# Kernel optimization log

Measured on AMD Instinct MI355X. Metric: run time of the kernel, lower is better.

Reference implementation:

```python
import jax, jax.numpy as jnp
import numpy as np
import math

N_HEADS = 32
N_KV_HEADS = 8
HEAD_DIM = 64
ROPE_BASE = 10000.0


def _rope_cos_sin(L, dtype):
    # inv_freq: [head_dim/2]
    inv_freq = 1.0 / (ROPE_BASE ** (jnp.arange(0, HEAD_DIM, 2, dtype=jnp.float32) / HEAD_DIM))
    t = jnp.arange(L, dtype=jnp.float32)
    freqs = jnp.outer(t, inv_freq)            # [L, head_dim/2]
    emb = jnp.concatenate([freqs, freqs], -1)  # [L, head_dim]
    return jnp.cos(emb).astype(dtype), jnp.sin(emb).astype(dtype)


def _rotate_half(x):
    x1, x2 = jnp.split(x, 2, axis=-1)
    return jnp.concatenate([-x2, x1], axis=-1)


def setup_inputs() -> dict:
    key = jax.random.key(0)
    ks = jax.random.split(key, 5)
    B, L, D = 2, 2048, 2048
    s = 0.02
    return {
        "x": jax.random.normal(ks[0], (B, L, D), jnp.float32),
        "Wq": jax.random.normal(ks[1], (D, N_HEADS * HEAD_DIM), jnp.float32) * s,
        "Wk": jax.random.normal(ks[2], (D, N_KV_HEADS * HEAD_DIM), jnp.float32) * s,
        "Wv": jax.random.normal(ks[3], (D, N_KV_HEADS * HEAD_DIM), jnp.float32) * s,
        "Wo": jax.random.normal(ks[4], (N_HEADS * HEAD_DIM, D), jnp.float32) * s,
    }


def reference(x, Wq, Wk, Wv, Wo):
    B, L, D = x.shape
    G = N_HEADS // N_KV_HEADS
    # QKV projections -> [B, H, L, hd]
    q = (x @ Wq).reshape(B, L, N_HEADS, HEAD_DIM).transpose(0, 2, 1, 3)
    k = (x @ Wk).reshape(B, L, N_KV_HEADS, HEAD_DIM).transpose(0, 2, 1, 3)
    v = (x @ Wv).reshape(B, L, N_KV_HEADS, HEAD_DIM).transpose(0, 2, 1, 3)
    # RoPE
    cos, sin = _rope_cos_sin(L, x.dtype)  # [L, hd]
    cos = cos[None, None]
    sin = sin[None, None]
    q = q * cos + _rotate_half(q) * sin
    k = k * cos + _rotate_half(k) * sin
    # GQA expand kv heads (repeat_interleave along head dim)
    k = jnp.repeat(k, G, axis=1)
    v = jnp.repeat(v, G, axis=1)
    # Causal SDPA
    scale = 1.0 / math.sqrt(HEAD_DIM)
    scores = jnp.einsum('bhqd,bhkd->bhqk', q, k) * scale  # [B,H,L,L]
    causal = jnp.tril(jnp.ones((L, L), bool))
    scores = jnp.where(causal[None, None], scores, jnp.finfo(scores.dtype).min)
    probs = jax.nn.softmax(scores, axis=-1)
    out = jnp.einsum('bhqk,bhkd->bhqd', probs, v)  # [B,H,L,hd]
    out = out.transpose(0, 2, 1, 3).reshape(B, L, N_HEADS * HEAD_DIM)
    return out @ Wo
```

## Files before the change

### kernel.cpp

```cpp
#include <hip/hip_runtime.h>
#include <hip/hip_bf16.h>
#include <stdint.h>

typedef __bf16 bf16_t;
typedef bf16_t bf16x2 __attribute__((ext_vector_type(2)));
typedef bf16_t bf16x4 __attribute__((ext_vector_type(4)));
typedef bf16_t bf16x8 __attribute__((ext_vector_type(8)));
typedef float f32x4 __attribute__((ext_vector_type(4)));
typedef float f32x16 __attribute__((ext_vector_type(16)));

#define NH 32
#define NKV 8
#define HD 64
#define LSEQ 2048
#define DMODEL 2048
#define BATCH 2

#define QSCALE 0.18033688011112042f
#define DEFER_THR 11.5f

__device__ __forceinline__ void gl_lds16(const void* g, void* l) {
  __builtin_amdgcn_global_load_lds(
      (__attribute__((address_space(1))) char*)(uintptr_t)g,
      (__attribute__((address_space(3))) char*)(uintptr_t)l, 16, 0, 0);
}

__device__ __forceinline__ unsigned pack2(float a, float b) {
  bf16x2 t;
  t[0] = (bf16_t)a;
  t[1] = (bf16_t)b;
  return __builtin_bit_cast(unsigned, t);
}


__global__ void cvt_x(const float4* __restrict__ s, bf16x4* __restrict__ d, int n4) {
  int i = blockIdx.x * blockDim.x + threadIdx.x;
  if (i >= n4) return;
  float4 v = s[i];
  bf16x4 o;
  o[0] = (bf16_t)v.x; o[1] = (bf16_t)v.y; o[2] = (bf16_t)v.z; o[3] = (bf16_t)v.w;
  d[i] = o;
}

__global__ void transpose_w(const float* __restrict__ W, bf16_t* __restrict__ WT,
                            int K, int N) {
  __shared__ float tile[32][33];
  int nb = blockIdx.x * 32, kb = blockIdx.y * 32;
  int tx = threadIdx.x, ty = threadIdx.y;
#pragma unroll
  for (int i = 0; i < 32; i += 8)
    tile[ty + i][tx] = W[(size_t)(kb + ty + i) * N + nb + tx];
  __syncthreads();
#pragma unroll
  for (int i = 0; i < 32; i += 8)
    WT[(size_t)(nb + ty + i) * K + kb + tx] = (bf16_t)tile[tx][ty + i];
}

__global__ void rope_table(float* __restrict__ cosT, float* __restrict__ sinT) {
  int t = blockIdx.x * blockDim.x + threadIdx.x;
  int l = t >> 5, i = t & 31;
  float inv = powf(10000.0f, -(float)i / 32.0f);
  float ang = (float)l * inv;
  float s, c;
  sincosf(ang, &s, &c);
  cosT[t] = c;
  sinT[t] = s;
}

template <int EPI>
__global__ __launch_bounds__(256, 3) void gemm128(
    const bf16_t* __restrict__ A, const bf16_t* __restrict__ BT,
    float* __restrict__ Cf, bf16_t* __restrict__ Qo, bf16_t* __restrict__ Ko,
    bf16_t* __restrict__ Vo, int M, int N, int K,
    const float* __restrict__ cosT, const float* __restrict__ sinT, int nx) {
  __shared__ bf16_t Al[128 * 64];
  __shared__ bf16_t Bl[128 * 64];
  const int tid = threadIdx.x, lane = tid & 63, w = tid >> 6;
  const int wm = w >> 1, wn = w & 1;
  const int r15 = lane & 15, g = lane >> 4;
  const int nwg = (int)gridDim.x;
  const int sid = ((int)blockIdx.x & 7) * (nwg >> 3) + ((int)blockIdx.x >> 3);
  const int m0 = (sid / nx) * 128, n0 = (sid % nx) * 128;
  f32x4 acc[4][4] = {};

  for (int kt = 0; kt < K; kt += 64) {
#pragma unroll
    for (int i = 0; i < 4; ++i) {
      const int c = i * 256 + tid;
      const int row = c >> 3, cc = c & 7;
      const int sc = (cc ^ (row & 7)) * 8;
      gl_lds16(A + (size_t)(m0 + row) * K + kt + sc, Al + c * 8);
      gl_lds16(BT + (size_t)(n0 + row) * K + kt + sc, Bl + c * 8);
    }
    __syncthreads();
#pragma unroll
    for (int kk = 0; kk < 2; ++kk) {
      bf16x8 af[4], bfr[4];
#pragma unroll
      for (int mi = 0; mi < 4; ++mi) {
        const int r = wm * 64 + mi * 16 + r15;
        af[mi] = *(const bf16x8*)((const char*)Al + r * 128 +
                                  (((kk * 4 + g) ^ (r & 7)) << 4));
      }
#pragma unroll
      for (int ni = 0; ni < 4; ++ni) {
        const int r = wn * 64 + ni * 16 + r15;
        bfr[ni] = *(const bf16x8*)((const char*)Bl + r * 128 +
                                   (((kk * 4 + g) ^ (r & 7)) << 4));
      }
#pragma unroll
      for (int mi = 0; mi < 4; ++mi)
#pragma unroll
        for (int ni = 0; ni < 4; ++ni)
          acc[mi][ni] = __builtin_amdgcn_mfma_f32_16x16x32_bf16(
              af[mi], bfr[ni], acc[mi][ni], 0, 0, 0);
    }
    __syncthreads();
  }

  if constexpr (EPI == 0) {
#pragma unroll
    for (int mi = 0; mi < 4; ++mi) {
      const int row = m0 + wm * 64 + mi * 16 + g * 4;
#pragma unroll
      for (int ni = 0; ni < 4; ++ni) {
        const int col = n0 + wn * 64 + ni * 16 + r15;
#pragma unroll
        for (int r = 0; r < 4; ++r)
          Cf[(size_t)(row + r) * N + col] = acc[mi][ni][r];
      }
    }
  } else {
    const int colbase = n0 + wn * 64;
    auto rope_store = [&](bf16_t* C, int NHT, int colrel, float sc) {
#pragma unroll
      for (int mi = 0; mi < 4; ++mi)
#pragma unroll
        for (int r = 0; r < 4; ++r) {
          const int rowg = m0 + wm * 64 + mi * 16 + g * 4 + r;
          const int bb = rowg >> 11, ls = rowg & (LSEQ - 1);
#pragma unroll
          for (int ni = 0; ni < 2; ++ni) {
            const int col = colrel + ni * 16 + r15;
            const int hh = col >> 6, d = col & 63;
            const float c = cosT[ls * 32 + d], s = sinT[ls * 32 + d];
            const float v0 = acc[mi][ni][r], v1 = acc[mi][ni + 2][r];
            bf16_t* dst = C + (((size_t)bb * NHT + hh) * LSEQ + ls) * HD + d;
            dst[0] = (bf16_t)((v0 * c - v1 * s) * sc);
            dst[32] = (bf16_t)((v1 * c + v0 * s) * sc);
          }
        }
    };
    if (n0 < 2048) {
      rope_store(Qo, NH, colbase, QSCALE);
    } else if (n0 < 2560) {
      rope_store(Ko, NKV, colbase - 2048, 1.0f);
    } else {
#pragma unroll
      for (int mi = 0; mi < 4; ++mi)
#pragma unroll
        for (int r = 0; r < 4; ++r) {
          const int rowg = m0 + wm * 64 + mi * 16 + g * 4 + r;
          const int bb = rowg >> 11, ls = rowg & (LSEQ - 1);
#pragma unroll
          for (int ni = 0; ni < 4; ++ni) {
            const int col = colbase - 2560 + ni * 16 + r15;
            const int hh = col >> 6, d = col & 63;
            Vo[(((size_t)bb * NKV + hh) * HD + d) * LSEQ + ls] =
                (bf16_t)acc[mi][ni][r];
          }
        }
    }
  }
}

__global__ __launch_bounds__(256, 2) void attn_fwd(
    const bf16_t* __restrict__ Q, const bf16_t* __restrict__ Kh,
    const bf16_t* __restrict__ VTh, bf16_t* __restrict__ AO) {
  __shared__ bf16_t Kl[2][64 * 64];
  __shared__ bf16_t Vl[2][64 * 64];
  const int tid = threadIdx.x, lane = tid & 63, w = tid >> 6;
  const int col = lane & 31, hi = lane >> 5;
  const int pairid = blockIdx.x;
  const int hk = blockIdx.y, b = blockIdx.z;
  const int h = hk * 4 + w;

  const bf16_t* Qh_ = Q + ((size_t)b * NH + h) * LSEQ * HD;
  const bf16_t* Kb = Kh + ((size_t)b * NKV + hk) * LSEQ * HD;
  const bf16_t* Vb = VTh + ((size_t)b * NKV + hk) * HD * LSEQ;

  auto stage = [&](int buf, int kt) {
#pragma unroll
    for (int i = 0; i < 2; ++i) {
      const int c = i * 256 + tid;
      const int row = c >> 3, cc = c & 7;
      const int scol = (cc ^ (row & 7)) * 16;
      gl_lds16((const char*)Kb + (size_t)(kt * 64 + row) * 128 + scol,
               (char*)&Kl[buf][0] + c * 16);
      gl_lds16((const char*)Vb + (size_t)row * 4096 + (size_t)kt * 128 + scol,
               (char*)&Vl[buf][0] + c * 16);
    }
  };

  int cur = 0;
  for (int p = 0; p < 2; ++p) {
    const int qt = p ? pairid : 63 - pairid;
    const int nt = (qt >> 1) + 1;
    const int qoff = (qt & 1) * 32;
    const bf16_t* Qb = Qh_ + (size_t)qt * 32 * HD;

    bf16x8 qf[4];
#pragma unroll
    for (int kc = 0; kc < 4; ++kc)
      qf[kc] = *(const bf16x8*)&Qb[(size_t)col * HD + kc * 16 + hi * 8];

    f32x16 o[2] = {};
    float m = -1e30f, lsum = 0.f;

    stage(cur, 0);
    __syncthreads();
    for (int kt = 0; kt < nt; ++kt) {
      if (kt + 1 < nt) stage(cur ^ 1, kt + 1);
      const bool diag = (kt == nt - 1);

      f32x16 sfrag[2] = {};
#pragma unroll
      for (int kvs = 0; kvs < 2; ++kvs) {
        if (diag && kvs * 32 > 31 + qoff) {
#pragma unroll
          for (int r = 0; r < 16; ++r) sfrag[kvs][r] = -1e30f;
          continue;
        }
        bf16x8 ak[4];
#pragma unroll
        for (int kc = 0; kc < 4; ++kc) {
          const int row = kvs * 32 + col;
          const int slot = ((kc * 2 + hi) ^ (row & 7)) * 16;
          ak[kc] = *(const bf16x8*)((const char*)&Kl[cur][0] + row * 128 + slot);
        }
#pragma unroll
        for (int kc = 0; kc < 4; ++kc)
          sfrag[kvs] = __builtin_amdgcn_mfma_f32_32x32x16_bf16(
              ak[kc], qf[kc], sfrag[kvs], 0, 0, 0);
      }

      if (diag) {
#pragma unroll
        for (int kvs = 0; kvs < 2; ++kvs)
#pragma unroll
          for (int r = 0; r < 16; ++r) {
            const int kvl = kvs * 32 + (r & 3) + 8 * (r >> 2) + 4 * hi;
            if (kvl > col + qoff) sfrag[kvs][r] = -1e30f;
          }
      }

      float mx = sfrag[0][0];
#pragma unroll
      for (int r = 1; r < 16; ++r) mx = fmaxf(mx, sfrag[0][r]);
#pragma unroll
      for (int r = 0; r < 16; ++r) mx = fmaxf(mx, sfrag[1][r]);
      mx = fmaxf(mx, __shfl_xor(mx, 32));

      if (__any(mx > m + DEFER_THR)) {
        const float mn = fmaxf(m, mx);
        const float al = __builtin_amdgcn_exp2f(m - mn);
        lsum *= al;
        m = mn;
#pragma unroll
        for (int ds = 0; ds < 2; ++ds)
#pragma unroll
          for (int r = 0; r < 16; ++r) o[ds][r] *= al;
      }

      bf16x8 pf[4];
#pragma unroll
      for (int kvs = 0; kvs < 2; ++kvs)
#pragma unroll
        for (int c1 = 0; c1 < 2; ++c1) {
          float pv[8];
#pragma unroll
          for (int j = 0; j < 8; ++j) {
            pv[j] = __builtin_amdgcn_exp2f(sfrag[kvs][c1 * 8 + j] - m);
            lsum += pv[j];
          }
          const unsigned a01 = pack2(pv[0], pv[1]), a23 = pack2(pv[2], pv[3]);
          const unsigned b01 = pack2(pv[4], pv[5]), b23 = pack2(pv[6], pv[7]);
          const unsigned s01 = __shfl_xor(hi ? a01 : b01, 32);
          const unsigned s23 = __shfl_xor(hi ? a23 : b23, 32);
          union { unsigned u[4]; bf16x8 v; } t;
          t.u[0] = hi ? s01 : a01;
          t.u[1] = hi ? s23 : a23;
          t.u[2] = hi ? b01 : s01;
          t.u[3] = hi ? b23 : s23;
          pf[kvs * 2 + c1] = t.v;
        }

#pragma unroll
      for (int ds = 0; ds < 2; ++ds) {
        bf16x8 av[4];
#pragma unroll
        for (int kc2 = 0; kc2 < 4; ++kc2) {
          const int row = ds * 32 + col;
          const int slot = ((kc2 * 2 + hi) ^ (row & 7)) * 16;
          av[kc2] = *(const bf16x8*)((const char*)&Vl[cur][0] + row * 128 + slot);
        }
#pragma unroll
        for (int kc2 = 0; kc2 < 4; ++kc2) {
          if (diag && kc2 * 16 > 31 + qoff) continue;
          o[ds] = __builtin_amdgcn_mfma_f32_32x32x16_bf16(
              av[kc2], pf[kc2], o[ds], 0, 0, 0);
        }
      }

      __syncthreads();
      cur ^= 1;
    }

    lsum += __shfl_xor(lsum, 32);
    const float inv = 1.0f / lsum;
    const int q = qt * 32 + col;
#pragma unroll
    for (int ds = 0; ds < 2; ++ds)
#pragma unroll
      for (int g4 = 0; g4 < 4; ++g4) {
        bf16x4 o4;
#pragma unroll
        for (int j = 0; j < 4; ++j) o4[j] = (bf16_t)(o[ds][g4 * 4 + j] * inv);
        const int d = ds * 32 + 8 * g4 + 4 * hi;
        *(bf16x4*)&AO[((size_t)b * LSEQ + q) * DMODEL + h * HD + d] = o4;
      }
  }
}


extern "C" void kernel_launch(void* const* d_in, const int* in_sizes, int n_in,
                              void* d_out, int out_size, void* d_ws, size_t ws_size,
                              hipStream_t stream) {
  const float* x = (const float*)d_in[0];
  const float* Wq = (const float*)d_in[1];
  const float* Wk = (const float*)d_in[2];
  const float* Wv = (const float*)d_in[3];
  const float* Wo = (const float*)d_in[4];
  char* ws = (char*)d_ws;
  size_t off = 0;
  auto alloc = [&](size_t bytes) {
    char* p = ws + off;
    off += (bytes + 255) & ~(size_t)255;
    return p;
  };
  bf16_t* xb = (bf16_t*)alloc((size_t)BATCH * LSEQ * DMODEL * 2);
  bf16_t* wqkvT = (bf16_t*)alloc((size_t)3072 * DMODEL * 2);
  bf16_t* wot = (bf16_t*)alloc((size_t)DMODEL * DMODEL * 2);
  float* cosT = (float*)alloc((size_t)LSEQ * 32 * 4);
  float* sinT = (float*)alloc((size_t)LSEQ * 32 * 4);
  bf16_t* Qh = (bf16_t*)alloc((size_t)BATCH * NH * LSEQ * HD * 2);
  bf16_t* Kh = (bf16_t*)alloc((size_t)BATCH * NKV * LSEQ * HD * 2);
  bf16_t* VTh = (bf16_t*)alloc((size_t)BATCH * NKV * HD * LSEQ * 2);
  bf16_t* AO = (bf16_t*)alloc((size_t)BATCH * LSEQ * NH * HD * 2);
  (void)ws_size; (void)in_sizes; (void)n_in; (void)out_size;

  const int M = BATCH * LSEQ;

  cvt_x<<<(M * DMODEL / 4 + 255) / 256, 256, 0, stream>>>(
      (const float4*)x, (bf16x4*)xb, M * DMODEL / 4);
  transpose_w<<<dim3(64, 64), dim3(32, 8), 0, stream>>>(Wq, wqkvT, 2048, 2048);
  transpose_w<<<dim3(16, 64), dim3(32, 8), 0, stream>>>(
      Wk, wqkvT + (size_t)2048 * 2048, 2048, 512);
  transpose_w<<<dim3(16, 64), dim3(32, 8), 0, stream>>>(
      Wv, wqkvT + (size_t)2560 * 2048, 2048, 512);
  transpose_w<<<dim3(64, 64), dim3(32, 8), 0, stream>>>(Wo, wot, 2048, 2048);
  rope_table<<<LSEQ * 32 / 256, 256, 0, stream>>>(cosT, sinT);

  gemm128<3><<<768, 256, 0, stream>>>(
      xb, wqkvT, nullptr, Qh, Kh, VTh, M, 3072, 2048, cosT, sinT, 24);

  attn_fwd<<<dim3(32, NKV, BATCH), 256, 0, stream>>>(Qh, Kh, VTh, AO);

  gemm128<0><<<512, 256, 0, stream>>>(
      AO, wot, (float*)d_out, nullptr, nullptr, nullptr, M, 2048, 2048,
      nullptr, nullptr, 16);
}
```

Baseline: 181.0 us.

## Deepen attention KV pipeline to 4-stage ring and compute row sums via MFMA

Replaces the double-buffered K/V LDS staging with a four-slot ring that prefetches two tiles ahead. Each iteration uses explicit vmcnt waits and a single barrier instead of the end-of-loop __syncthreads. The softmax denominator is now computed by an extra MFMA with a ones vector, replacing per-element scalar adds. This doubles LDS use (64KB per block), which may limit the two-blocks-per-CU occupancy, and the hand-counted vmcnt values must match the number of outstanding loads.

```diff
diff --git a/kernel.cpp b/kernel.cpp
--- a/kernel.cpp
+++ b/kernel.cpp
@@ -177,8 +177,8 @@
 __global__ __launch_bounds__(256, 2) void attn_fwd(
     const bf16_t* __restrict__ Q, const bf16_t* __restrict__ Kh,
     const bf16_t* __restrict__ VTh, bf16_t* __restrict__ AO) {
-  __shared__ bf16_t Kl[2][64 * 64];
-  __shared__ bf16_t Vl[2][64 * 64];
+  __shared__ bf16_t Kl[4][64 * 64];
+  __shared__ bf16_t Vl[4][64 * 64];
   const int tid = threadIdx.x, lane = tid & 63, w = tid >> 6;
   const int col = lane & 31, hi = lane >> 5;
   const int pairid = blockIdx.x;
@@ -188,6 +188,10 @@
   const bf16_t* Qh_ = Q + ((size_t)b * NH + h) * LSEQ * HD;
   const bf16_t* Kb = Kh + ((size_t)b * NKV + hk) * LSEQ * HD;
   const bf16_t* Vb = VTh + ((size_t)b * NKV + hk) * HD * LSEQ;
+
+  bf16x8 ones8;
+#pragma unroll
+  for (int j = 0; j < 8; ++j) ones8[j] = (bf16_t)1.0f;
 
   auto stage = [&](int buf, int kt) {
 #pragma unroll
@@ -202,7 +206,6 @@
     }
   };
 
-  int cur = 0;
   for (int p = 0; p < 2; ++p) {
     const int qt = p ? pairid : 63 - pairid;
     const int nt = (qt >> 1) + 1;
@@ -215,12 +218,24 @@
       qf[kc] = *(const bf16x8*)&Qb[(size_t)col * HD + kc * 16 + hi * 8];
 
     f32x16 o[2] = {};
-    float m = -1e30f, lsum = 0.f;
-
-    stage(cur, 0);
-    __syncthreads();
+    f32x16 osum = {};
+    float m = -1e30f;
+
+    stage(0, 0);
+    if (nt > 1) stage(1, 1);
     for (int kt = 0; kt < nt; ++kt) {
-      if (kt + 1 < nt) stage(cur ^ 1, kt + 1);
+      if (kt + 2 < nt) {
+        stage((kt + 2) & 3, kt + 2);
+        asm volatile("s_waitcnt vmcnt(8)" ::: "memory");
+      } else if (kt + 1 < nt) {
+        asm volatile("s_waitcnt vmcnt(4)" ::: "memory");
+      } else {
+        asm volatile("s_waitcnt vmcnt(0)" ::: "memory");
+      }
+      __builtin_amdgcn_s_barrier();
+      __builtin_amdgcn_sched_barrier(0);
+      const char* Kcur = (const char*)&Kl[kt & 3][0];
+      const char* Vcur = (const char*)&Vl[kt & 3][0];
       const bool diag = (kt == nt - 1);
 
       f32x16 sfrag[2] = {};
@@ -236,7 +251,7 @@
         for (int kc = 0; kc < 4; ++kc) {
           const int row = kvs * 32 + col;
           const int slot = ((kc * 2 + hi) ^ (row & 7)) * 16;
-          ak[kc] = *(const bf16x8*)((const char*)&Kl[cur][0] + row * 128 + slot);
+          ak[kc] = *(const bf16x8*)(Kcur + row * 128 + slot);
         }
 #pragma unroll
         for (int kc = 0; kc < 4; ++kc)
@@ -264,8 +279,9 @@
       if (__any(mx > m + DEFER_THR)) {
         const float mn = fmaxf(m, mx);
         const float al = __builtin_amdgcn_exp2f(m - mn);
-        lsum *= al;
         m = mn;
+#pragma unroll
+        for (int r = 0; r < 16; ++r) osum[r] *= al;
 #pragma unroll
         for (int ds = 0; ds < 2; ++ds)
 #pragma unroll
@@ -279,10 +295,8 @@
         for (int c1 = 0; c1 < 2; ++c1) {
           float pv[8];
 #pragma unroll
-          for (int j = 0; j < 8; ++j) {
+          for (int j = 0; j < 8; ++j)
             pv[j] = __builtin_amdgcn_exp2f(sfrag[kvs][c1 * 8 + j] - m);
-            lsum += pv[j];
-          }
           const unsigned a01 = pack2(pv[0], pv[1]), a23 = pack2(pv[2], pv[3]);
           const unsigned b01 = pack2(pv[4], pv[5]), b23 = pack2(pv[6], pv[7]);
           const unsigned s01 = __shfl_xor(hi ? a01 : b01, 32);
@@ -302,7 +316,7 @@
         for (int kc2 = 0; kc2 < 4; ++kc2) {
           const int row = ds * 32 + col;
           const int slot = ((kc2 * 2 + hi) ^ (row & 7)) * 16;
-          av[kc2] = *(const bf16x8*)((const char*)&Vl[cur][0] + row * 128 + slot);
+          av[kc2] = *(const bf16x8*)(Vcur + row * 128 + slot);
         }
 #pragma unroll
         for (int kc2 = 0; kc2 < 4; ++kc2) {
@@ -311,13 +325,15 @@
               av[kc2], pf[kc2], o[ds], 0, 0, 0);
         }
       }
-
-      __syncthreads();
-      cur ^= 1;
-    }
-
-    lsum += __shfl_xor(lsum, 32);
-    const float inv = 1.0f / lsum;
+#pragma unroll
+      for (int kc2 = 0; kc2 < 4; ++kc2) {
+        if (diag && kc2 * 16 > 31 + qoff) continue;
+        osum = __builtin_amdgcn_mfma_f32_32x32x16_bf16(
+            ones8, pf[kc2], osum, 0, 0, 0);
+      }
+    }
+
+    const float inv = 1.0f / osum[0];
     const int q = qt * 32 + col;
 #pragma unroll
     for (int ds = 0; ds < 2; ++ds)
@@ -329,6 +345,7 @@
         const int d = ds * 32 + 8 * g4 + 4 * hi;
         *(bf16x4*)&AO[((size_t)b * LSEQ + q) * DMODEL + h * HD + d] = o4;
       }
+    __builtin_amdgcn_s_barrier();
   }
 }
 
```

New measurement: 183.6 us. About the same (+1.5%).
